# Kernel tuning notes

Hardware: AMD Instinct MI355X
Metric: run time of the kernel (lower is better)

The kernel has to match this reference:

```python
import jax, jax.numpy as jnp
import numpy as np

# dims: batch B, tokens T, model_dim D, expert hidden H, experts E, top-k K
B, T, D, H, E, K = 4, 2048, 2048, 2048, 8, 2
CAP_FACTOR = 1.0
S = B * T
C = int(np.ceil(K * S / E * CAP_FACTOR))  # per-expert capacity = 2048


def setup_inputs() -> dict:
    key = jax.random.key(0)
    k0, k1, k2, k3 = jax.random.split(key, 4)
    x = jax.random.normal(k0, (B, T, D), dtype=jnp.float32)
    wg = jax.random.normal(k1, (D, E), dtype=jnp.float32) * (D ** -0.5)
    w1 = jax.random.normal(k2, (E, D, H), dtype=jnp.float32) * (D ** -0.5)
    b1 = jnp.zeros((E, H), dtype=jnp.float32)
    w2 = jax.random.normal(k3, (E, H, D), dtype=jnp.float32) * (H ** -0.5)
    b2 = jnp.zeros((E, D), dtype=jnp.float32)
    return {"x": x, "wg": wg, "w1": w1, "b1": b1, "w2": w2, "b2": b2}


def _moe(x, wg, w1, b1, w2, b2):
    xt = x.reshape(S, D)
    # --- top-k gating (deepspeed-style, gates normalized over selected k) ---
    gates = jax.nn.softmax(xt @ wg, axis=-1)            # [S,E]
    vals, idx = jax.lax.top_k(gates, K)                 # [S,K]
    vals = vals / jnp.sum(vals, axis=-1, keepdims=True)
    # --- capacity-aware slot assignment (slot j offset by counts of slots < j) ---
    m = jax.nn.one_hot(idx, E, dtype=jnp.int32).transpose(1, 0, 2)  # [K,S,E]
    within = jnp.cumsum(m, axis=1) - m                  # 0-based rank within expert per slot
    counts = jnp.sum(m, axis=1)                         # [K,E]
    offs = jnp.cumsum(counts, axis=0) - counts          # [K,E] offsets from earlier slots
    loc = jnp.sum((within + offs[:, None, :]) * m, axis=2)  # [K,S]
    eid = idx.T                                         # [K,S]
    valid = loc < C
    loc_c = jnp.minimum(loc, C - 1)
    # --- dispatch: scatter raw tokens into [E,C,D] expert buffers ---
    contrib = jnp.where(valid[..., None], xt[None, :, :], 0.0)   # [K,S,D]
    disp = jnp.zeros((E, C, D), x.dtype).at[eid, loc_c].add(contrib)
    # --- grouped expert FFN: relu(x @ W1 + b1) @ W2 + b2 ---
    h = jax.nn.relu(jnp.einsum('ecd,edh->ech', disp, w1) + b1[:, None, :])
    ye = jnp.einsum('ech,ehd->ecd', h, w2) + b2[:, None, :]
    # --- combine: gather expert outputs, weight by normalized gates ---
    gathered = ye[eid, loc_c]                           # [K,S,D]
    w = (vals.T * valid).astype(x.dtype)                # [K,S]
    out = jnp.einsum('ks,ksd->sd', w, gathered)
    return out.reshape(B, T, D)


def reference(x, wg, w1, b1, w2, b2):
    y = _moe(x, wg, w1, b1, w2, b2)                     # [B,T,D]
    return jax.nn.log_softmax(jnp.sum(y, axis=2), axis=1)  # [B,T]
```

## Files before the change

### kernel.cpp

```cpp
#include <hip/hip_runtime.h>
#include <math.h>

#define S_TOK 8192
#define DDIM 2048
#define HDIM 2048
#define NE 8
#define CAP 2048
#define NBATCH 4
#define TT 2048

typedef _Float16 f16;
typedef _Float16 f16x4 __attribute__((ext_vector_type(4)));
typedef _Float16 f16x8 __attribute__((ext_vector_type(8)));
typedef float f32x4 __attribute__((ext_vector_type(4)));

typedef __attribute__((address_space(1))) const void* gas_ptr;
typedef __attribute__((address_space(3))) void* las_ptr;

__global__ __launch_bounds__(256) void gating_kernel(const float* __restrict__ x,
                                                     const float* __restrict__ wg,
                                                     int* __restrict__ eid,
                                                     float* __restrict__ wts,
                                                     int* __restrict__ slot_token,
                                                     float* __restrict__ zacc) {
  if (blockIdx.x < 64) {
    int i = blockIdx.x * 256 + threadIdx.x;
    slot_token[i] = 0;
    zacc[i] = 0.f;
  }
  int wid = threadIdx.x >> 6;
  int lane = threadIdx.x & 63;
  int s = blockIdx.x * 4 + wid;
  const float* xr = x + (size_t)s * DDIM;
  double acc[8];
#pragma unroll
  for (int e = 0; e < 8; ++e) acc[e] = 0.0;
  for (int d0 = 0; d0 < DDIM; d0 += 64) {
    float xs = xr[d0 + lane];
    const float4* wp = (const float4*)(wg + (size_t)(d0 + lane) * 8);
    float4 g0 = wp[0];
    float4 g1 = wp[1];
    double xd = (double)xs;
    acc[0] += xd * (double)g0.x; acc[1] += xd * (double)g0.y;
    acc[2] += xd * (double)g0.z; acc[3] += xd * (double)g0.w;
    acc[4] += xd * (double)g1.x; acc[5] += xd * (double)g1.y;
    acc[6] += xd * (double)g1.z; acc[7] += xd * (double)g1.w;
  }
#pragma unroll
  for (int e = 0; e < 8; ++e) {
    double v = acc[e];
    for (int off = 32; off > 0; off >>= 1) v += __shfl_down(v, off, 64);
    acc[e] = v;
  }
  if (lane == 0) {
    int e0 = 0; double l0 = acc[0];
    for (int e = 1; e < 8; ++e) if (acc[e] > l0) { l0 = acc[e]; e0 = e; }
    int e1 = -1; double l1 = -1e300;
    for (int e = 0; e < 8; ++e) if (e != e0 && acc[e] > l1) { l1 = acc[e]; e1 = e; }
    double pe = exp(l1 - l0);
    double inv = 1.0 / (1.0 + pe);
    eid[2 * s] = e0; eid[2 * s + 1] = e1;
    wts[2 * s] = (float)inv; wts[2 * s + 1] = (float)(pe * inv);
  }
}

__global__ __launch_bounds__(256) void scan_kernel(const int* __restrict__ eid,
                                                   int* __restrict__ locb,
                                                   int* __restrict__ slot_token) {
  __shared__ int seg[4][2][8];
  __shared__ int base[4][2][8];
  int tid = threadIdx.x, wid = tid >> 6, lane = tid & 63;
  unsigned long long lower = (lane == 0) ? 0ull : ((~0ull) >> (64 - lane));
  const int2* eid2 = (const int2*)eid;
  int c0 = 0, c1 = 0;
  for (int r = 0; r < 32; ++r) {
    int2 ee = eid2[wid * 2048 + r * 64 + lane];
#pragma unroll
    for (int e = 0; e < 8; ++e) {
      unsigned long long b0 = __ballot(ee.x == e);
      unsigned long long b1 = __ballot(ee.y == e);
      if (lane == e) { c0 += __popcll(b0); c1 += __popcll(b1); }
    }
  }
  if (lane < 8) { seg[wid][0][lane] = c0; seg[wid][1][lane] = c1; }
  __syncthreads();
  if (lane < 8) {
    int e = lane;
    int tot0 = seg[0][0][e] + seg[1][0][e] + seg[2][0][e] + seg[3][0][e];
    int b0 = 0, b1 = tot0;
    for (int w = 0; w < wid; ++w) { b0 += seg[w][0][e]; b1 += seg[w][1][e]; }
    base[wid][0][e] = b0; base[wid][1][e] = b1;
  }
  for (int r = 0; r < 32; ++r) {
    int2 ee = eid2[wid * 2048 + r * 64 + lane];
    int rank0 = 0, rank1 = 0, add0 = 0, add1 = 0;
#pragma unroll
    for (int e = 0; e < 8; ++e) {
      unsigned long long b0 = __ballot(ee.x == e);
      unsigned long long b1 = __ballot(ee.y == e);
      if (ee.x == e) rank0 = __popcll(b0 & lower);
      if (ee.y == e) rank1 = __popcll(b1 & lower);
      if (lane == e) { add0 = __popcll(b0); add1 = __popcll(b1); }
    }
    int loc0 = base[wid][0][ee.x] + rank0;
    int loc1 = base[wid][1][ee.y] + rank1;
    int s = wid * 2048 + r * 64 + lane;
    int2 lo; lo.x = loc0; lo.y = loc1;
    *(int2*)&locb[2 * s] = lo;
    if (loc0 < CAP) slot_token[ee.x * CAP + loc0] = s;
    if (loc1 < CAP) slot_token[ee.y * CAP + loc1] = s;
    if (lane < 8) {
      atomicAdd(&base[wid][0][lane], add0);
      atomicAdd(&base[wid][1][lane], add1);
    }
  }
}

#define W1T_BLOCKS 8192
#define W2S_BLOCKS 4096
#define ABUILD_BASE (W1T_BLOCKS + W2S_BLOCKS + 1)
__global__ __launch_bounds__(256) void prep_kernel(const float* __restrict__ w1,
                                                   const float* __restrict__ w2,
                                                   const float* __restrict__ b2,
                                                   const float* __restrict__ x,
                                                   const int* __restrict__ slot_token,
                                                   f16* __restrict__ W1T,
                                                   float* __restrict__ w2s,
                                                   float* __restrict__ b2s,
                                                   f16* __restrict__ A16) {
  __shared__ float tile[64 * 65];
  int bid = blockIdx.x, tid = threadIdx.x;
  if (bid >= ABUILD_BASE) {
    int slot = bid - ABUILD_BASE;
    int s = slot_token[slot];
    const float4* x4 = (const float4*)x + (size_t)s * 512;
    f16x4* outp = (f16x4*)(A16 + (size_t)slot * DDIM);
#pragma unroll
    for (int i = 0; i < 2; ++i) {
      int v = i * 256 + tid;
      float4 xv = x4[v];
      f16x4 h;
      h[0] = (f16)xv.x; h[1] = (f16)xv.y; h[2] = (f16)xv.z; h[3] = (f16)xv.w;
      outp[v] = h;
    }
    return;
  }
  if (bid < W1T_BLOCKS) {
    int e = bid >> 10, rem = bid & 1023;
    int d0 = (rem >> 5) << 6;
    int h0 = (rem & 31) << 6;
    const float* w1e = w1 + (size_t)e * DDIM * HDIM;
#pragma unroll
    for (int i = 0; i < 4; ++i) {
      int linear = i * 256 + tid;
      int r = linear >> 4, c4 = linear & 15;
      float4 v = *(const float4*)(w1e + (size_t)(d0 + r) * HDIM + h0 + c4 * 4);
      float* t = &tile[r * 65 + c4 * 4];
      t[0] = v.x; t[1] = v.y; t[2] = v.z; t[3] = v.w;
    }
    __syncthreads();
    f16* W1Te = W1T + (size_t)e * HDIM * DDIM;
#pragma unroll
    for (int i = 0; i < 2; ++i) {
      int linear = i * 256 + tid;
      int hr = linear >> 3, l8 = linear & 7;
      f16x8 o;
#pragma unroll
      for (int j = 0; j < 8; ++j) o[j] = (f16)tile[(l8 * 8 + j) * 65 + hr];
      *(f16x8*)(W1Te + (size_t)(h0 + hr) * DDIM + d0 + l8 * 8) = o;
    }
    return;
  }
  if (bid < W1T_BLOCKS + W2S_BLOCKS) {
    int wid = tid >> 6, lane = tid & 63;
    int row = (bid - W1T_BLOCKS) * 4 + wid;
    const float4* w24 = (const float4*)w2;
    float acc = 0.f;
    for (int j = 0; j < 8; ++j) {
      float4 v = w24[(size_t)row * 512 + j * 64 + lane];
      acc += v.x + v.y + v.z + v.w;
    }
    for (int off = 32; off > 0; off >>= 1) acc += __shfl_down(acc, off, 64);
    if (lane == 0) w2s[row] = acc;
    return;
  }
  {
    int e = tid >> 5, l32 = tid & 31;
    float acc = 0.f;
    for (int j = 0; j < 64; ++j) acc += b2[e * 2048 + j * 32 + l32];
    for (int off = 16; off > 0; off >>= 1) acc += __shfl_down(acc, off, 32);
    if (l32 == 0) b2s[e] = acc;
  }
}

__global__ __launch_bounds__(256) void gemm_kernel(const f16* __restrict__ A16,
                                                   const f16* __restrict__ W1T,
                                                   const float* __restrict__ b1,
                                                   const float* __restrict__ w2s,
                                                   float* __restrict__ zacc) {
  __shared__ __align__(16) f16 As[128 * 32];
  __shared__ __align__(16) f16 Bs[128 * 32];
  int tid = threadIdx.x;
  int wid = tid >> 6, lane = tid & 63;
  int bid = blockIdx.x;
  int e = bid >> 8;
  int r = bid & 255;
  int st = r >> 4, wi = r & 15;
  int cT = (st >> 2) * 4 + (wi >> 2);
  int hT = (st & 3) * 4 + (wi & 3);
  int c0 = cT * 128, h0 = hT * 128;
  const f16* Abase = A16 + ((size_t)e * CAP + c0) * DDIM;
  const f16* Bbase = W1T + ((size_t)e * HDIM + h0) * DDIM;
  f32x4 acc[4][4];
#pragma unroll
  for (int i = 0; i < 4; ++i)
#pragma unroll
    for (int j = 0; j < 4; ++j) acc[i][j] = (f32x4){0.f, 0.f, 0.f, 0.f};
  int wm = (wid >> 1) * 64, wn = (wid & 1) * 64;
  int quad = lane >> 4, l15 = lane & 15;

  const f16* Aln = Abase + (size_t)(wid * 32 + (lane >> 2)) * DDIM + (lane & 3) * 8;
  const f16* Bln = Bbase + (size_t)(wid * 32 + (lane >> 2)) * DDIM + (lane & 3) * 8;
  f16* ldsA0 = &As[wid * 1024];
  f16* ldsA1 = &As[wid * 1024 + 512];
  f16* ldsB0 = &Bs[wid * 1024];
  f16* ldsB1 = &Bs[wid * 1024 + 512];

  for (int k0 = 0; k0 < DDIM; k0 += 32) {
    __syncthreads();
    __builtin_amdgcn_global_load_lds((gas_ptr)(Aln + k0), (las_ptr)ldsA0, 16, 0, 0);
    __builtin_amdgcn_global_load_lds((gas_ptr)(Aln + k0 + 16 * DDIM), (las_ptr)ldsA1, 16, 0, 0);
    __builtin_amdgcn_global_load_lds((gas_ptr)(Bln + k0), (las_ptr)ldsB0, 16, 0, 0);
    __builtin_amdgcn_global_load_lds((gas_ptr)(Bln + k0 + 16 * DDIM), (las_ptr)ldsB1, 16, 0, 0);
    __syncthreads();
    f16x8 af[4], bfr[4];
#pragma unroll
    for (int mt = 0; mt < 4; ++mt)
      af[mt] = *(const f16x8*)&As[(wm + mt * 16 + l15) * 32 + quad * 8];
#pragma unroll
    for (int nt = 0; nt < 4; ++nt)
      bfr[nt] = *(const f16x8*)&Bs[(wn + nt * 16 + l15) * 32 + quad * 8];
#pragma unroll
    for (int mt = 0; mt < 4; ++mt)
#pragma unroll
      for (int nt = 0; nt < 4; ++nt)
        acc[mt][nt] = __builtin_amdgcn_mfma_f32_16x16x32_f16(af[mt], bfr[nt], acc[mt][nt], 0, 0, 0);
  }
  float b1v[4], wsv[4];
#pragma unroll
  for (int nt = 0; nt < 4; ++nt) {
    int h = h0 + wn + nt * 16 + l15;
    b1v[nt] = b1[e * HDIM + h];
    wsv[nt] = w2s[e * HDIM + h];
  }
#pragma unroll
  for (int mt = 0; mt < 4; ++mt) {
    float pr[4];
#pragma unroll
    for (int rr = 0; rr < 4; ++rr) {
      float t = 0.f;
#pragma unroll
      for (int nt = 0; nt < 4; ++nt) {
        float v = acc[mt][nt][rr] + b1v[nt];
        t += (v > 0.f ? v : 0.f) * wsv[nt];
      }
      pr[rr] = t;
    }
#pragma unroll
    for (int rr = 0; rr < 4; ++rr)
#pragma unroll
      for (int off = 1; off < 16; off <<= 1) pr[rr] += __shfl_xor(pr[rr], off, 64);
    if (l15 == 0) {
      int m = c0 + wm + mt * 16 + quad * 4;
#pragma unroll
      for (int rr = 0; rr < 4; ++rr) atomicAdd(&zacc[e * CAP + m + rr], pr[rr]);
    }
  }
}

__global__ __launch_bounds__(256) void tail_kernel(const int* __restrict__ eid,
                                                   const int* __restrict__ locb,
                                                   const float* __restrict__ wts,
                                                   const float* __restrict__ zacc,
                                                   const float* __restrict__ b2s,
                                                   float* __restrict__ out) {
  __shared__ float red[4];
  int b = blockIdx.x, tid = threadIdx.x;
  int wid = tid >> 6, lane = tid & 63;
  float v[8];
  float mx = -1e30f;
#pragma unroll
  for (int i = 0; i < 8; ++i) {
    int s = b * TT + i * 256 + tid;
    float zz = 0.f;
#pragma unroll
    for (int k = 0; k < 2; ++k) {
      int e = eid[2 * s + k], loc = locb[2 * s + k];
      if (loc < CAP) zz += wts[2 * s + k] * (zacc[e * CAP + loc] + b2s[e]);
    }
    v[i] = zz;
    mx = fmaxf(mx, zz);
  }
  for (int off = 32; off > 0; off >>= 1) mx = fmaxf(mx, __shfl_xor(mx, off, 64));
  if (lane == 0) red[wid] = mx;
  __syncthreads();
  mx = fmaxf(fmaxf(red[0], red[1]), fmaxf(red[2], red[3]));
  float sum = 0.f;
#pragma unroll
  for (int i = 0; i < 8; ++i) sum += expf(v[i] - mx);
  for (int off = 32; off > 0; off >>= 1) sum += __shfl_xor(sum, off, 64);
  __syncthreads();
  if (lane == 0) red[wid] = sum;
  __syncthreads();
  sum = red[0] + red[1] + red[2] + red[3];
  float lse = mx + logf(sum);
#pragma unroll
  for (int i = 0; i < 8; ++i) out[b * TT + i * 256 + tid] = v[i] - lse;
}

extern "C" void kernel_launch(void* const* d_in, const int* in_sizes, int n_in,
                              void* d_out, int out_size, void* d_ws, size_t ws_size,
                              hipStream_t stream) {
  const float* x  = (const float*)d_in[0];
  const float* wg = (const float*)d_in[1];
  const float* w1 = (const float*)d_in[2];
  const float* b1 = (const float*)d_in[3];
  const float* w2 = (const float*)d_in[4];
  const float* b2 = (const float*)d_in[5];
  float* out = (float*)d_out;

  char* ws = (char*)d_ws;
  size_t off = 0;
  auto alloc = [&](size_t bytes) -> char* {
    char* p = ws + off;
    off += (bytes + 255) & ~(size_t)255;
    return p;
  };
  f16* A16 = (f16*)alloc((size_t)NE * CAP * DDIM * 2);
  f16* W1T = (f16*)alloc((size_t)NE * HDIM * DDIM * 2);
  float* w2s = (float*)alloc((size_t)NE * HDIM * 4);
  float* b2s = (float*)alloc(NE * 4);
  int* eid = (int*)alloc((size_t)S_TOK * 2 * 4);
  float* wts = (float*)alloc((size_t)S_TOK * 2 * 4);
  int* locb = (int*)alloc((size_t)S_TOK * 2 * 4);
  int* slot_token = (int*)alloc((size_t)NE * CAP * 4);
  float* zacc = (float*)alloc((size_t)NE * CAP * 4);
  if (off > ws_size) return;

  gating_kernel<<<S_TOK / 4, 256, 0, stream>>>(x, wg, eid, wts, slot_token, zacc);
  scan_kernel<<<1, 256, 0, stream>>>(eid, locb, slot_token);
  prep_kernel<<<ABUILD_BASE + NE * CAP, 256, 0, stream>>>(w1, w2, b2, x, slot_token,
                                                          W1T, w2s, b2s, A16);
  gemm_kernel<<<NE * 256, 256, 0, stream>>>(A16, W1T, b1, w2s, zacc);
  tail_kernel<<<NBATCH, 256, 0, stream>>>(eid, locb, wts, zacc, b2s, out);
}
```

Baseline: 592.0 us.

## Rewrite expert GEMM with 256x256 tiles, double-buffered LDS and swizzled layout

After: 545.8 us. -7.8%, faster.

```diff
diff --git a/kernel.cpp b/kernel.cpp
--- a/kernel.cpp
+++ b/kernel.cpp
@@ -193,76 +193,208 @@
   }
 }
 
-__global__ __launch_bounds__(256) void gemm_kernel(const f16* __restrict__ A16,
-                                                   const f16* __restrict__ W1T,
-                                                   const float* __restrict__ b1,
-                                                   const float* __restrict__ w2s,
-                                                   float* __restrict__ zacc) {
-  __shared__ __align__(16) f16 As[128 * 32];
-  __shared__ __align__(16) f16 Bs[128 * 32];
-  int tid = threadIdx.x;
-  int wid = tid >> 6, lane = tid & 63;
+
+template <int MB, int NB>
+__device__ __forceinline__ void quad_mfma(f32x4 (&acc)[8][4], const f16x8 (&av)[4][2],
+                                          const f16x8 (&bv)[2][2]) {
+#pragma unroll
+  for (int mf = 0; mf < 4; ++mf)
+#pragma unroll
+    for (int nf = 0; nf < 2; ++nf) {
+      f32x4 c = acc[MB + mf][NB + nf];
+      c = __builtin_amdgcn_mfma_f32_16x16x32_f16(av[mf][0], bv[nf][0], c, 0, 0, 0);
+      c = __builtin_amdgcn_mfma_f32_16x16x32_f16(av[mf][1], bv[nf][1], c, 0, 0, 0);
+      acc[MB + mf][NB + nf] = c;
+    }
+}
+
+__device__ __forceinline__ void lda4(f16x8 (&av)[4][2], const f16* p0, const f16* p1, int mh) {
+#pragma unroll
+  for (int mf = 0; mf < 4; ++mf) {
+    av[mf][0] = *(const f16x8*)(p0 + (mh * 4 + mf) * 1024);
+    av[mf][1] = *(const f16x8*)(p1 + (mh * 4 + mf) * 1024);
+  }
+}
+__device__ __forceinline__ void ldb2(f16x8 (&bv)[2][2], const f16* p0, const f16* p1, int nh) {
+#pragma unroll
+  for (int nf = 0; nf < 2; ++nf) {
+    bv[nf][0] = *(const f16x8*)(p0 + (nh * 2 + nf) * 1024);
+    bv[nf][1] = *(const f16x8*)(p1 + (nh * 2 + nf) * 1024);
+  }
+}
+
+__device__ __forceinline__ void stage_half(const f16* tile_rows, f16* lds_region,
+                                           int T, int h, int wl8, int wu8, int cs) {
+#pragma unroll
+  for (int i = 0; i < 2; ++i) {
+    const f16* g = tile_rows + (size_t)(h * 128 + i * 64 + wl8) * DDIM + T * 64 + cs * 8;
+    f16* d = lds_region + (h * 128 + i * 64 + wu8) * 64;
+    __builtin_amdgcn_global_load_lds((gas_ptr)g, (las_ptr)d, 16, 0, 0);
+  }
+}
+
+__device__ __forceinline__ void bar() {
+  asm volatile("" ::: "memory");
+  __builtin_amdgcn_s_barrier();
+  asm volatile("" ::: "memory");
+}
+__device__ __forceinline__ void mfma_open() {
+  bar();
+  asm volatile("s_waitcnt lgkmcnt(0)" ::: "memory");
+  __builtin_amdgcn_sched_barrier(0);
+  __builtin_amdgcn_s_setprio(1);
+}
+__device__ __forceinline__ void mfma_close() {
+  __builtin_amdgcn_s_setprio(0);
+  bar();
+}
+__device__ __forceinline__ void mfma_close_w4() {
+  __builtin_amdgcn_s_setprio(0);
+  asm volatile("s_waitcnt vmcnt(4)" ::: "memory");
+  bar();
+}
+__device__ __forceinline__ void mfma_close_w0() {
+  __builtin_amdgcn_s_setprio(0);
+  asm volatile("s_waitcnt vmcnt(0)" ::: "memory");
+  bar();
+}
+
+__global__ __launch_bounds__(512, 2) void gemm_kernel(const f16* __restrict__ A16,
+                                                      const f16* __restrict__ W1T,
+                                                      const float* __restrict__ b1,
+                                                      const float* __restrict__ w2s,
+                                                      float* __restrict__ zacc) {
+  __shared__ __align__(16) f16 lds[4 * 256 * 64];
+  const int tid = threadIdx.x;
+  const int wid = tid >> 6, lane = tid & 63;
+  const int wm = wid >> 2, wn = wid & 3;
+  const int quad = lane >> 4, l15 = lane & 15;
+  const int l3 = lane >> 3, c7 = lane & 7;
+  const int cs = c7 ^ l3;
+  const int wl8 = wid * 8 + l3, wu8 = wid * 8;
+
   int bid = blockIdx.x;
-  int e = bid >> 8;
-  int r = bid & 255;
-  int st = r >> 4, wi = r & 15;
-  int cT = (st >> 2) * 4 + (wi >> 2);
-  int hT = (st & 3) * 4 + (wi & 3);
-  int c0 = cT * 128, h0 = hT * 128;
+  int e = bid & 7;
+  int idx = bid >> 3;
+  int cT = idx >> 3, hT = idx & 7;
+  int c0 = cT * 256, h0 = hT * 256;
+
   const f16* Abase = A16 + ((size_t)e * CAP + c0) * DDIM;
   const f16* Bbase = W1T + ((size_t)e * HDIM + h0) * DDIM;
-  f32x4 acc[4][4];
-#pragma unroll
-  for (int i = 0; i < 4; ++i)
-#pragma unroll
-    for (int j = 0; j < 4; ++j) acc[i][j] = (f32x4){0.f, 0.f, 0.f, 0.f};
-  int wm = (wid >> 1) * 64, wn = (wid & 1) * 64;
-  int quad = lane >> 4, l15 = lane & 15;
-
-  const f16* Aln = Abase + (size_t)(wid * 32 + (lane >> 2)) * DDIM + (lane & 3) * 8;
-  const f16* Bln = Bbase + (size_t)(wid * 32 + (lane >> 2)) * DDIM + (lane & 3) * 8;
-  f16* ldsA0 = &As[wid * 1024];
-  f16* ldsA1 = &As[wid * 1024 + 512];
-  f16* ldsB0 = &Bs[wid * 1024];
-  f16* ldsB1 = &Bs[wid * 1024 + 512];
-
-  for (int k0 = 0; k0 < DDIM; k0 += 32) {
-    __syncthreads();
-    __builtin_amdgcn_global_load_lds((gas_ptr)(Aln + k0), (las_ptr)ldsA0, 16, 0, 0);
-    __builtin_amdgcn_global_load_lds((gas_ptr)(Aln + k0 + 16 * DDIM), (las_ptr)ldsA1, 16, 0, 0);
-    __builtin_amdgcn_global_load_lds((gas_ptr)(Bln + k0), (las_ptr)ldsB0, 16, 0, 0);
-    __builtin_amdgcn_global_load_lds((gas_ptr)(Bln + k0 + 16 * DDIM), (las_ptr)ldsB1, 16, 0, 0);
-    __syncthreads();
-    f16x8 af[4], bfr[4];
-#pragma unroll
-    for (int mt = 0; mt < 4; ++mt)
-      af[mt] = *(const f16x8*)&As[(wm + mt * 16 + l15) * 32 + quad * 8];
-#pragma unroll
-    for (int nt = 0; nt < 4; ++nt)
-      bfr[nt] = *(const f16x8*)&Bs[(wn + nt * 16 + l15) * 32 + quad * 8];
-#pragma unroll
-    for (int mt = 0; mt < 4; ++mt)
-#pragma unroll
-      for (int nt = 0; nt < 4; ++nt)
-        acc[mt][nt] = __builtin_amdgcn_mfma_f32_16x16x32_f16(af[mt], bfr[nt], acc[mt][nt], 0, 0, 0);
-  }
+
+  f16* bufA0 = &lds[0];
+  f16* bufB0 = &lds[16384];
+  f16* bufA1 = &lds[2 * 16384];
+  f16* bufB1 = &lds[3 * 16384];
+
+  const int so0 = (quad ^ c7) * 8;
+  const int so1 = ((quad + 4) ^ c7) * 8;
+  const f16* a0k0 = bufA0 + (wm * 128 + l15) * 64 + so0;
+  const f16* a0k1 = bufA0 + (wm * 128 + l15) * 64 + so1;
+  const f16* a1k0 = a0k0 + 2 * 16384;
+  const f16* a1k1 = a0k1 + 2 * 16384;
+  const f16* b0k0 = bufB0 + (wn * 64 + l15) * 64 + so0;
+  const f16* b0k1 = bufB0 + (wn * 64 + l15) * 64 + so1;
+  const f16* b1k0 = b0k0 + 2 * 16384;
+  const f16* b1k1 = b0k1 + 2 * 16384;
+
+  f32x4 acc[8][4];
+#pragma unroll
+  for (int i = 0; i < 8; ++i)
+#pragma unroll
+    for (int jj = 0; jj < 4; ++jj) acc[i][jj] = (f32x4){0.f, 0.f, 0.f, 0.f};
+  f16x8 fa[4][2], fb0[2][2], fb1[2][2];
+
+  stage_half(Abase, bufA0, 0, 0, wl8, wu8, cs);
+  stage_half(Abase, bufA0, 0, 1, wl8, wu8, cs);
+  stage_half(Bbase, bufB0, 0, 0, wl8, wu8, cs);
+  stage_half(Bbase, bufB0, 0, 1, wl8, wu8, cs);
+  stage_half(Bbase, bufB1, 1, 0, wl8, wu8, cs);
+  stage_half(Bbase, bufB1, 1, 1, wl8, wu8, cs);
+  asm volatile("s_waitcnt vmcnt(4)" ::: "memory");
+  bar();
+
+#pragma unroll 1
+  for (int it = 0; it < 15; ++it) {
+    const int Ta = 2 * it + 1, Tb = 2 * it + 2, Tc = 2 * it + 3;
+    lda4(fa, a0k0, a0k1, 0);
+    ldb2(fb0, b0k0, b0k1, 0);
+    stage_half(Abase, bufA1, Ta, 0, wl8, wu8, cs);
+    mfma_open(); quad_mfma<0, 0>(acc, fa, fb0); mfma_close();
+
+    ldb2(fb1, b0k0, b0k1, 1);
+    stage_half(Abase, bufA1, Ta, 1, wl8, wu8, cs);
+    mfma_open(); quad_mfma<0, 2>(acc, fa, fb1); mfma_close();
+
+    lda4(fa, a0k0, a0k1, 1);
+    stage_half(Bbase, bufB0, Tb, 0, wl8, wu8, cs);
+    mfma_open(); quad_mfma<4, 2>(acc, fa, fb1); mfma_close();
+
+    stage_half(Bbase, bufB0, Tb, 1, wl8, wu8, cs);
+    mfma_open(); quad_mfma<4, 0>(acc, fa, fb0); mfma_close_w4();
+
+    lda4(fa, a1k0, a1k1, 0);
+    ldb2(fb0, b1k0, b1k1, 0);
+    stage_half(Abase, bufA0, Tb, 0, wl8, wu8, cs);
+    mfma_open(); quad_mfma<0, 0>(acc, fa, fb0); mfma_close();
+
+    ldb2(fb1, b1k0, b1k1, 1);
+    stage_half(Abase, bufA0, Tb, 1, wl8, wu8, cs);
+    mfma_open(); quad_mfma<0, 2>(acc, fa, fb1); mfma_close();
+
+    lda4(fa, a1k0, a1k1, 1);
+    stage_half(Bbase, bufB1, Tc, 0, wl8, wu8, cs);
+    mfma_open(); quad_mfma<4, 2>(acc, fa, fb1); mfma_close();
+
+    stage_half(Bbase, bufB1, Tc, 1, wl8, wu8, cs);
+    mfma_open(); quad_mfma<4, 0>(acc, fa, fb0); mfma_close_w4();
+  }
+  {
+    lda4(fa, a0k0, a0k1, 0);
+    ldb2(fb0, b0k0, b0k1, 0);
+    stage_half(Abase, bufA1, 31, 0, wl8, wu8, cs);
+    mfma_open(); quad_mfma<0, 0>(acc, fa, fb0); mfma_close();
+
+    ldb2(fb1, b0k0, b0k1, 1);
+    stage_half(Abase, bufA1, 31, 1, wl8, wu8, cs);
+    mfma_open(); quad_mfma<0, 2>(acc, fa, fb1); mfma_close();
+
+    lda4(fa, a0k0, a0k1, 1);
+    mfma_open(); quad_mfma<4, 2>(acc, fa, fb1); mfma_close();
+
+    mfma_open(); quad_mfma<4, 0>(acc, fa, fb0); mfma_close_w0();
+
+    lda4(fa, a1k0, a1k1, 0);
+    ldb2(fb0, b1k0, b1k1, 0);
+    mfma_open(); quad_mfma<0, 0>(acc, fa, fb0); mfma_close();
+
+    ldb2(fb1, b1k0, b1k1, 1);
+    mfma_open(); quad_mfma<0, 2>(acc, fa, fb1); mfma_close();
+
+    lda4(fa, a1k0, a1k1, 1);
+    mfma_open(); quad_mfma<4, 2>(acc, fa, fb1); mfma_close();
+
+    mfma_open(); quad_mfma<4, 0>(acc, fa, fb0);
+    __builtin_amdgcn_s_setprio(0);
+  }
+
   float b1v[4], wsv[4];
 #pragma unroll
-  for (int nt = 0; nt < 4; ++nt) {
-    int h = h0 + wn + nt * 16 + l15;
-    b1v[nt] = b1[e * HDIM + h];
-    wsv[nt] = w2s[e * HDIM + h];
-  }
-#pragma unroll
-  for (int mt = 0; mt < 4; ++mt) {
+  for (int nf = 0; nf < 4; ++nf) {
+    int h = h0 + wn * 64 + nf * 16 + l15;
+    b1v[nf] = b1[e * HDIM + h];
+    wsv[nf] = w2s[e * HDIM + h];
+  }
+#pragma unroll
+  for (int mf = 0; mf < 8; ++mf) {
     float pr[4];
 #pragma unroll
     for (int rr = 0; rr < 4; ++rr) {
       float t = 0.f;
 #pragma unroll
-      for (int nt = 0; nt < 4; ++nt) {
-        float v = acc[mt][nt][rr] + b1v[nt];
-        t += (v > 0.f ? v : 0.f) * wsv[nt];
+      for (int nf = 0; nf < 4; ++nf) {
+        float v = acc[mf][nf][rr] + b1v[nf];
+        t += (v > 0.f ? v : 0.f) * wsv[nf];
       }
       pr[rr] = t;
     }
@@ -271,7 +403,7 @@
 #pragma unroll
       for (int off = 1; off < 16; off <<= 1) pr[rr] += __shfl_xor(pr[rr], off, 64);
     if (l15 == 0) {
-      int m = c0 + wm + mt * 16 + quad * 4;
+      int m = c0 + wm * 128 + mf * 16 + quad * 4;
 #pragma unroll
       for (int rr = 0; rr < 4; ++rr) atomicAdd(&zacc[e * CAP + m + rr], pr[rr]);
     }
@@ -351,6 +483,6 @@
   scan_kernel<<<1, 256, 0, stream>>>(eid, locb, slot_token);
   prep_kernel<<<ABUILD_BASE + NE * CAP, 256, 0, stream>>>(w1, w2, b2, x, slot_token,
                                                           W1T, w2s, b2s, A16);
-  gemm_kernel<<<NE * 256, 256, 0, stream>>>(A16, W1T, b1, w2s, zacc);
+  gemm_kernel<<<NE * 64, 512, 0, stream>>>(A16, W1T, b1, w2s, zacc);
   tail_kernel<<<NBATCH, 256, 0, stream>>>(eid, locb, wts, zacc, b2s, out);
 }
```
